# Kernel optimization log

Measured on AMD Instinct MI355X. Metric: run time of the kernel, lower is better.

Reference implementation:

```python
import jax, jax.numpy as jnp
import numpy as np

IN_DIM = 128
OUT_DIM = 128
H = 8
HD = OUT_DIM // H  # 16
EPS = 1e-5
NEG = -1e30


def setup_inputs() -> dict:
    key = jax.random.key(0)
    ks = jax.random.split(key, 10)
    B, N = 8, 1024
    h = jax.random.normal(ks[0], (B, N, IN_DIM), dtype=jnp.float32)
    adj_mask = jax.random.randint(ks[1], (B, N, N), 0, 2, dtype=jnp.int32)
    s = 1.0 / np.sqrt(IN_DIM)
    W = jax.random.normal(ks[2], (H, IN_DIM, HD), dtype=jnp.float32) * s
    a = jax.random.normal(ks[3], (H, 2 * HD), dtype=jnp.float32) * (1.0 / np.sqrt(2 * HD))
    ln1_g = jnp.ones((OUT_DIM,), jnp.float32)
    ln1_b = jnp.zeros((OUT_DIM,), jnp.float32)
    w1 = jax.random.normal(ks[4], (OUT_DIM, 2 * OUT_DIM), dtype=jnp.float32) * (1.0 / np.sqrt(OUT_DIM))
    b1 = jnp.zeros((2 * OUT_DIM,), jnp.float32)
    w2 = jax.random.normal(ks[5], (2 * OUT_DIM, OUT_DIM), dtype=jnp.float32) * (1.0 / np.sqrt(2 * OUT_DIM))
    b2 = jnp.zeros((OUT_DIM,), jnp.float32)
    ln2_g = jnp.ones((OUT_DIM,), jnp.float32)
    ln2_b = jnp.zeros((OUT_DIM,), jnp.float32)
    return dict(h=h, adj_mask=adj_mask, W=W, a=a, ln1_g=ln1_g, ln1_b=ln1_b,
                w1=w1, b1=b1, w2=w2, b2=b2, ln2_g=ln2_g, ln2_b=ln2_b)


def _layernorm(x, g, b):
    mu = jnp.mean(x, axis=-1, keepdims=True)
    var = jnp.mean(jnp.square(x - mu), axis=-1, keepdims=True)
    return (x - mu) * jax.lax.rsqrt(var + EPS) * g + b


def reference(h, adj_mask, W, a, ln1_g, ln1_b, w1, b1, w2, b2, ln2_g, ln2_b):
    B, N, _ = h.shape
    # Per-head projection: (B,H,N,HD)
    Wh = jnp.einsum('bni,hid->bhnd', h, W)
    # a.[Wh_i, Wh_j] = a_src.Wh_i + a_dst.Wh_j (decompose concat-score)
    a_src, a_dst = a[:, :HD], a[:, HD:]
    s_i = jnp.einsum('bhnd,hd->bhn', Wh, a_src)  # source term
    s_j = jnp.einsum('bhnd,hd->bhn', Wh, a_dst)  # target term
    e = s_i[:, :, :, None] + s_j[:, :, None, :]  # (B,H,N,N)
    e = jnp.where(e >= 0, e, 0.2 * e)            # LeakyReLU(0.2)
    mask = (adj_mask != 0)[:, None, :, :]        # (B,1,N,N)
    e = jnp.where(mask, e, NEG)
    alpha = jax.nn.softmax(e, axis=-1)
    # rows with no neighbors -> NaN in torch softmax -> zeroed; replicate
    row_valid = jnp.any(mask, axis=-1, keepdims=True)  # (B,1,N,1)
    alpha = jnp.where(row_valid, alpha, 0.0)
    # dropout in eval mode = identity
    h_heads = jnp.einsum('bhnm,bhmd->bhnd', alpha, Wh)
    h_cat = h_heads.transpose(0, 2, 1, 3).reshape(B, N, H * HD)
    # residual (in_dim == out_dim here)
    h_cat = _layernorm(h_cat + h, ln1_g, ln1_b)
    ffn = jnp.maximum(h_cat @ w1 + b1, 0.0) @ w2 + b2
    return _layernorm(h_cat + ffn, ln2_g, ln2_b)
```

## Files before the change

kernel.cpp:

```cpp
#include <hip/hip_runtime.h>
#include <hip/hip_bf16.h>

#define IN_DIM 128
#define OUT_DIM 128
#define NHEAD 8
#define HD 16
#define BB 8
#define NN 1024
#define LOG2E 1.44269504f

typedef unsigned long long u64;
typedef float f32x4 __attribute__((ext_vector_type(4)));
typedef short bf16x8 __attribute__((ext_vector_type(8)));

__global__ __launch_bounds__(256) void k_prep(
    const float* __restrict__ hin, const float* __restrict__ W,
    const float* __restrict__ a, const int* __restrict__ adj,
    unsigned* __restrict__ bits_t, unsigned short* __restrict__ whT,
    float* __restrict__ si_g, float* __restrict__ sj_g,
    const float* __restrict__ w1, const float* __restrict__ w2,
    unsigned short* __restrict__ w1T, unsigned short* __restrict__ w2T)
{
    __shared__ float smem[32 * 132];
    int blk = blockIdx.x;
    int t = threadIdx.x;

    if (blk < 256) {
        int b = blk >> 5, ntile = blk & 31;
        const float* hrow = hin + ((size_t)b * NN + ntile * 32) * IN_DIM;
#pragma unroll
        for (int it = 0; it < 4; ++it) {
            int g = t + 256 * it;
            int row = g >> 5, c4 = g & 31;
            float4 v = ((const float4*)hrow)[g];
            *(float4*)&smem[row * 132 + c4 * 4] = v;
        }
        __syncthreads();

        int d4 = t & 3;
        int hq = (t >> 2) & 7;
        int ngrp = t >> 5;
        float acc[4][4];
#pragma unroll
        for (int q = 0; q < 4; ++q)
#pragma unroll
            for (int dd = 0; dd < 4; ++dd) acc[q][dd] = 0.f;

        for (int i4 = 0; i4 < 32; ++i4) {
            float4 wf[4];
#pragma unroll
            for (int k = 0; k < 4; ++k)
                wf[k] = *(const float4*)&W[((size_t)hq * 128 + i4 * 4 + k) * 16 + d4 * 4];
            float4 hv[4];
#pragma unroll
            for (int q = 0; q < 4; ++q)
                hv[q] = *(const float4*)&smem[(ngrp * 4 + q) * 132 + i4 * 4];
#pragma unroll
            for (int q = 0; q < 4; ++q) {
                acc[q][0] += hv[q].x * wf[0].x + hv[q].y * wf[1].x + hv[q].z * wf[2].x + hv[q].w * wf[3].x;
                acc[q][1] += hv[q].x * wf[0].y + hv[q].y * wf[1].y + hv[q].z * wf[2].y + hv[q].w * wf[3].y;
                acc[q][2] += hv[q].x * wf[0].z + hv[q].y * wf[1].z + hv[q].z * wf[2].z + hv[q].w * wf[3].z;
                acc[q][3] += hv[q].x * wf[0].w + hv[q].y * wf[1].w + hv[q].z * wf[2].w + hv[q].w * wf[3].w;
            }
        }

        int bh = b * NHEAD + hq;
        int rowbase = ntile * 32 + ngrp * 4;

        float asrc[4], adst[4];
#pragma unroll
        for (int dd = 0; dd < 4; ++dd) {
            asrc[dd] = a[hq * 32 + d4 * 4 + dd];
            adst[dd] = a[hq * 32 + 16 + d4 * 4 + dd];
        }
#pragma unroll
        for (int q = 0; q < 4; ++q) {
            float psi = acc[q][0] * asrc[0] + acc[q][1] * asrc[1] + acc[q][2] * asrc[2] + acc[q][3] * asrc[3];
            float psj = acc[q][0] * adst[0] + acc[q][1] * adst[1] + acc[q][2] * adst[2] + acc[q][3] * adst[3];
            psi += __shfl_xor(psi, 1); psi += __shfl_xor(psi, 2);
            psj += __shfl_xor(psj, 1); psj += __shfl_xor(psj, 2);
            if (d4 == 0) {
                si_g[(size_t)bh * NN + rowbase + q] = psi * LOG2E;
                sj_g[(size_t)bh * NN + rowbase + q] = psj * LOG2E;
            }
        }

#pragma unroll
        for (int dd = 0; dd < 4; ++dd) {
            unsigned u0, u1;
            asm("v_cvt_pk_bf16_f32 %0, %1, %2" : "=v"(u0) : "v"(acc[0][dd]), "v"(acc[1][dd]));
            asm("v_cvt_pk_bf16_f32 %0, %1, %2" : "=v"(u1) : "v"(acc[2][dd]), "v"(acc[3][dd]));
            uint2 pk = make_uint2(u0, u1);
            *(uint2*)&whT[((size_t)bh * 16 + d4 * 4 + dd) * 1024 + rowbase] = pk;
        }
    } else if (blk < 2304) {
        int lane = t & 63;
        int wid = (blk - 256) * 4 + (t >> 6);
        for (int w = wid; w < BB * NN * 16; w += 2048 * 4) {
            int v = adj[(size_t)w * 64 + lane];
            u64 m = __ballot(v != 0);
            if (lane == 0) {
                int b = w >> 14, i = (w >> 4) & 1023, k = w & 15;
                unsigned* dst = bits_t + ((size_t)b * 32 + k * 2) * 1024 + i;
                dst[0] = (unsigned)m;
                dst[1024] = (unsigned)(m >> 32);
            }
        }
    } else {
        int bb = blk - 2304;
        const float* src; unsigned short* dst; int R, C;
        if (bb < 32) { src = w1; dst = w1T; R = 128; C = 256; }
        else         { src = w2; dst = w2T; R = 256; C = 128; bb -= 32; }
        int tpr = C >> 5;
        int tr = bb / tpr, tc = bb - tr * tpr;
        int r0 = tr << 5, c0 = tc << 5;
        int lr = t >> 5, lc = t & 31;
#pragma unroll
        for (int p = 0; p < 4; ++p)
            smem[(lr + p * 8) * 33 + lc] = src[(size_t)(r0 + lr + p * 8) * C + c0 + lc];
        __syncthreads();
#pragma unroll
        for (int p = 0; p < 4; ++p) {
            __hip_bfloat16 bv = __float2bfloat16(smem[lc * 33 + lr + p * 8]);
            dst[(size_t)(c0 + lr + p * 8) * R + r0 + lc] = *(unsigned short*)&bv;
        }
    }
}

__global__ __launch_bounds__(512, 3) void k_attn(
    const unsigned short* __restrict__ whT,
    const unsigned* __restrict__ bits_t,
    const float* __restrict__ si_g, const float* __restrict__ sj_g,
    float* __restrict__ hh)
{
    __shared__ __align__(16) unsigned short whT_s[16 * 1032];
    __shared__ __align__(16) float sj_s[NN];
    int t = threadIdx.x;
    int blk = blockIdx.x;
    int part = blk & 7;
    int bh = blk >> 3;
    int hq = bh & 7, b = bh >> 3;
    int blkrow = part * 128;

    {
        const uint4* src = (const uint4*)(whT + (size_t)bh * 16 * 1024);
#pragma unroll
        for (int it = 0; it < 4; ++it) {
            int g = t + 512 * it;
            int d = g >> 7, c8 = g & 127;
            uint4 v = src[g];
            *(uint4*)&whT_s[d * 1032 + c8 * 8] = v;
        }
        if (t < 256) *(float4*)&sj_s[t * 4] = ((const float4*)(sj_g + (size_t)bh * NN))[t];
    }
    __syncthreads();

    int wv = t >> 6, lane = t & 63;
    int lo16 = lane & 15, g = lane >> 4;
    int row = blkrow + wv * 16 + lo16;
    float si_r = si_g[(size_t)bh * NN + row];
    const unsigned* mcol = bits_t + (size_t)b * 32 * 1024 + row;

    f32x4 acc = {0.f, 0.f, 0.f, 0.f};
    float lsum = 0.f;
    unsigned m = mcol[0];
#pragma unroll 4
    for (int kt = 0; kt < 32; ++kt) {
        unsigned m_next = (kt < 31) ? mcol[(size_t)(kt + 1) * 1024] : 0u;
        bf16x8 bfrag = *(const bf16x8*)&whT_s[lo16 * 1032 + kt * 32 + g * 8];
        unsigned mm = m >> (g * 8);
        const float* sjp = &sj_s[kt * 32 + g * 8];
        union { bf16x8 v; unsigned u[4]; } af;
#pragma unroll
        for (int e2 = 0; e2 < 4; ++e2) {
            float v0 = si_r + sjp[2 * e2];
            float v1 = si_r + sjp[2 * e2 + 1];
            float lv0 = __builtin_fmaf(0.4f, __builtin_fabsf(v0), 0.6f * v0);
            float lv1 = __builtin_fmaf(0.4f, __builtin_fabsf(v1), 0.6f * v1);
            lv0 = ((mm >> (2 * e2)) & 1) ? lv0 : -150.f;
            lv1 = ((mm >> (2 * e2 + 1)) & 1) ? lv1 : -150.f;
            float p0, p1;
            asm("v_exp_f32 %0, %1" : "=v"(p0) : "v"(lv0));
            asm("v_exp_f32 %0, %1" : "=v"(p1) : "v"(lv1));
            lsum += p0 + p1;
            asm("v_cvt_pk_bf16_f32 %0, %1, %2" : "=v"(af.u[e2]) : "v"(p0), "v"(p1));
        }
        acc = __builtin_amdgcn_mfma_f32_16x16x32_bf16(af.v, bfrag, acc, 0, 0, 0);
        m = m_next;
    }

    lsum += __shfl_xor(lsum, 16);
    lsum += __shfl_xor(lsum, 32);

    float* obase = hh + ((size_t)b * NN + blkrow + wv * 16) * OUT_DIM + hq * HD + lo16;
#pragma unroll
    for (int q = 0; q < 4; ++q) {
        float ls = __shfl(lsum, 4 * g + q);
        float r = (ls > 0.f) ? 1.0f / ls : 0.f;
        obase[(size_t)(4 * g + q) * OUT_DIM] = acc[q] * r;
    }
}

__global__ __launch_bounds__(512, 1) void k_ffn(const float* __restrict__ hhs,
                                                const float* __restrict__ hin,
                                                const float* __restrict__ g1,
                                                const float* __restrict__ bt1,
                                                const unsigned short* __restrict__ w1T,
                                                const float* __restrict__ bb1,
                                                const unsigned short* __restrict__ w2T,
                                                const float* __restrict__ bb2,
                                                const float* __restrict__ g2,
                                                const float* __restrict__ bt2,
                                                float* __restrict__ out) {
    __shared__ float xc_f[32][128];
    __shared__ float y_f[32][132];
    __shared__ __align__(16) unsigned short xc_bf[32 * 128];
    __shared__ __align__(16) unsigned short hid_bf[32 * 256];

    int t = threadIdx.x;
    int R0 = blockIdx.x * 32;
    int wv = t >> 6, lane = t & 63;
    int lo = lane & 15, g = lane >> 4;

    bf16x8 b1f[2][4];
#pragma unroll
    for (int jt = 0; jt < 2; ++jt) {
        int n = (wv * 2 + jt) * 16 + lo;
#pragma unroll
        for (int kt = 0; kt < 4; ++kt)
            b1f[jt][kt] = *(const bf16x8*)&w1T[(size_t)n * 128 + kt * 32 + g * 8];
    }
    bf16x8 b2f[8];
    {
        int n = wv * 16 + lo;
#pragma unroll
        for (int kt = 0; kt < 8; ++kt)
            b2f[kt] = *(const bf16x8*)&w2T[(size_t)n * 256 + kt * 32 + g * 8];
    }
    float b1v[2];
    b1v[0] = bb1[(wv * 2 + 0) * 16 + lo];
    b1v[1] = bb1[(wv * 2 + 1) * 16 + lo];
    float b2v = bb2[wv * 16 + lo];

    {
        int r = t >> 4, c = t & 15;
        size_t row = (size_t)(R0 + r) * 128;
        float4 ha = *(const float4*)&hhs[row + c * 8];
        float4 hb = *(const float4*)&hhs[row + c * 8 + 4];
        float4 ia = *(const float4*)&hin[row + c * 8];
        float4 ib = *(const float4*)&hin[row + c * 8 + 4];
        float x[8] = {ha.x + ia.x, ha.y + ia.y, ha.z + ia.z, ha.w + ia.w,
                      hb.x + ib.x, hb.y + ib.y, hb.z + ib.z, hb.w + ib.w};
        float s = 0.f, s2 = 0.f;
#pragma unroll
        for (int j = 0; j < 8; ++j) { s += x[j]; s2 += x[j] * x[j]; }
#pragma unroll
        for (int off = 8; off > 0; off >>= 1) {
            s += __shfl_xor(s, off);
            s2 += __shfl_xor(s2, off);
        }
        float mu = s * (1.f / 128.f);
        float var = s2 * (1.f / 128.f) - mu * mu;
        float rs = rsqrtf(var + 1e-5f);
        float4 ga = *(const float4*)&g1[c * 8], gb = *(const float4*)&g1[c * 8 + 4];
        float4 ba = *(const float4*)&bt1[c * 8], bb = *(const float4*)&bt1[c * 8 + 4];
        float gg[8] = {ga.x, ga.y, ga.z, ga.w, gb.x, gb.y, gb.z, gb.w};
        float bbv[8] = {ba.x, ba.y, ba.z, ba.w, bb.x, bb.y, bb.z, bb.w};
        float xo[8];
#pragma unroll
        for (int j = 0; j < 8; ++j) xo[j] = (x[j] - mu) * rs * gg[j] + bbv[j];
        *(float4*)&xc_f[r][c * 8]     = make_float4(xo[0], xo[1], xo[2], xo[3]);
        *(float4*)&xc_f[r][c * 8 + 4] = make_float4(xo[4], xo[5], xo[6], xo[7]);
        union { uint4 v; unsigned u[4]; } pk;
#pragma unroll
        for (int q = 0; q < 4; ++q)
            asm("v_cvt_pk_bf16_f32 %0, %1, %2" : "=v"(pk.u[q]) : "v"(xo[2 * q]), "v"(xo[2 * q + 1]));
        int byte = (r * 256 + c * 16) ^ ((r & 7) << 4);
        *(uint4*)((char*)xc_bf + byte) = pk.v;
    }
    __syncthreads();

    {
        bf16x8 af[2][4];
#pragma unroll
        for (int mt = 0; mt < 2; ++mt) {
            int m = mt * 16 + lo;
#pragma unroll
            for (int kt = 0; kt < 4; ++kt) {
                int byte = (m * 256 + kt * 64 + g * 16) ^ ((m & 7) << 4);
                af[mt][kt] = *(const bf16x8*)((const char*)xc_bf + byte);
            }
        }
#pragma unroll
        for (int mt = 0; mt < 2; ++mt)
#pragma unroll
            for (int jt = 0; jt < 2; ++jt) {
                f32x4 acc = {0.f, 0.f, 0.f, 0.f};
#pragma unroll
                for (int kt = 0; kt < 4; ++kt)
                    acc = __builtin_amdgcn_mfma_f32_16x16x32_bf16(af[mt][kt], b1f[jt][kt], acc, 0, 0, 0);
                int n = (wv * 2 + jt) * 16 + lo;
#pragma unroll
                for (int q = 0; q < 4; ++q) {
                    float hv = fmaxf(acc[q] + b1v[jt], 0.f);
                    int m = mt * 16 + 4 * g + q;
                    int byte = (m * 512 + n * 2) ^ ((m & 7) << 4);
                    __hip_bfloat16 bv = __float2bfloat16(hv);
                    *(unsigned short*)((char*)hid_bf + byte) = *(unsigned short*)&bv;
                }
            }
    }
    __syncthreads();

    {
        f32x4 acc2[2] = {{0.f, 0.f, 0.f, 0.f}, {0.f, 0.f, 0.f, 0.f}};
#pragma unroll
        for (int mt = 0; mt < 2; ++mt) {
            int m = mt * 16 + lo;
#pragma unroll
            for (int kt = 0; kt < 8; ++kt) {
                int byte = (m * 512 + kt * 64 + g * 16) ^ ((m & 7) << 4);
                bf16x8 a = *(const bf16x8*)((const char*)hid_bf + byte);
                acc2[mt] = __builtin_amdgcn_mfma_f32_16x16x32_bf16(a, b2f[kt], acc2[mt], 0, 0, 0);
            }
        }
        int n = wv * 16 + lo;
#pragma unroll
        for (int mt = 0; mt < 2; ++mt)
#pragma unroll
            for (int q = 0; q < 4; ++q)
                y_f[mt * 16 + 4 * g + q][n] = acc2[mt][q] + b2v;
    }
    __syncthreads();

    {
        int r = t >> 4, c = t & 15;
        float xv[8];
        float s = 0.f, s2 = 0.f;
#pragma unroll
        for (int j = 0; j < 8; ++j) {
            float v = xc_f[r][c * 8 + j] + y_f[r][c * 8 + j];
            xv[j] = v; s += v; s2 += v * v;
        }
#pragma unroll
        for (int off = 8; off > 0; off >>= 1) {
            s += __shfl_xor(s, off);
            s2 += __shfl_xor(s2, off);
        }
        float mu = s * (1.f / 128.f);
        float var = s2 * (1.f / 128.f) - mu * mu;
        float rs = rsqrtf(var + 1e-5f);
        float4 ga = *(const float4*)&g2[c * 8], gb = *(const float4*)&g2[c * 8 + 4];
        float4 ba = *(const float4*)&bt2[c * 8], bb = *(const float4*)&bt2[c * 8 + 4];
        float o[8] = {(xv[0] - mu) * rs * ga.x + ba.x, (xv[1] - mu) * rs * ga.y + ba.y,
                      (xv[2] - mu) * rs * ga.z + ba.z, (xv[3] - mu) * rs * ga.w + ba.w,
                      (xv[4] - mu) * rs * gb.x + bb.x, (xv[5] - mu) * rs * gb.y + bb.y,
                      (xv[6] - mu) * rs * gb.z + bb.z, (xv[7] - mu) * rs * gb.w + bb.w};
        size_t row = (size_t)(R0 + r) * 128;
        *(float4*)&out[row + c * 8]     = make_float4(o[0], o[1], o[2], o[3]);
        *(float4*)&out[row + c * 8 + 4] = make_float4(o[4], o[5], o[6], o[7]);
    }
}

extern "C" void kernel_launch(void* const* d_in, const int* in_sizes, int n_in,
                              void* d_out, int out_size, void* d_ws, size_t ws_size,
                              hipStream_t stream) {
    const float* hin  = (const float*)d_in[0];
    const int*   adj  = (const int*)d_in[1];
    const float* W    = (const float*)d_in[2];
    const float* a    = (const float*)d_in[3];
    const float* ln1g = (const float*)d_in[4];
    const float* ln1b = (const float*)d_in[5];
    const float* w1   = (const float*)d_in[6];
    const float* b1   = (const float*)d_in[7];
    const float* w2   = (const float*)d_in[8];
    const float* b2   = (const float*)d_in[9];
    const float* ln2g = (const float*)d_in[10];
    const float* ln2b = (const float*)d_in[11];
    float* out = (float*)d_out;

    unsigned* bits_t    = (unsigned*)d_ws;
    unsigned short* whT = (unsigned short*)((char*)d_ws + (1u << 20));
    float* si_g         = (float*)((char*)d_ws + (3u << 20));
    float* sj_g         = (float*)((char*)d_ws + (3u << 20) + (256u << 10));
    float* hh           = (float*)((char*)d_ws + (3u << 20) + (512u << 10));
    unsigned short* w1T = (unsigned short*)((char*)d_ws + (7u << 20) + (512u << 10));
    unsigned short* w2T = (unsigned short*)((char*)d_ws + (7u << 20) + (512u << 10) + 65536);

    k_prep<<<2368, 256, 0, stream>>>(hin, W, a, adj, bits_t, whT, si_g, sj_g,
                                     w1, w2, w1T, w2T);
    k_attn<<<BB * NHEAD * 8, 512, 0, stream>>>(whT, bits_t, si_g, sj_g, hh);
    k_ffn<<<BB * NN / 32, 512, 0, stream>>>(hh, hin, ln1g, ln1b, w1T, b1, w2T, b2, ln2g, ln2b, out);
}
```

Baseline: 62.60 us.

## Factor LeakyReLU exponentials into per-row/per-column products and batch adjacency ballots

The attention kernel now precomputes exp(sj) and exp(0.2*sj) per column in shared memory and exp(si), exp(0.2*si) per row. Each score becomes max(e^si*e^sj, e^0.2si*e^0.2sj), which removes the per-element transcendental and the LeakyReLU arithmetic from the inner loop. The adjacency bit-packing loop also issues four independent loads and ballots per iteration so more memory accesses are in flight. The trade-offs are twice the shared-memory reads per element and a risk of overflow, since the exponentials are taken without subtracting a row maximum.

```diff
diff --git a/kernel.cpp b/kernel.cpp
--- a/kernel.cpp
+++ b/kernel.cpp
@@ -96,14 +96,31 @@
     } else if (blk < 2304) {
         int lane = t & 63;
         int wid = (blk - 256) * 4 + (t >> 6);
-        for (int w = wid; w < BB * NN * 16; w += 2048 * 4) {
-            int v = adj[(size_t)w * 64 + lane];
-            u64 m = __ballot(v != 0);
+#pragma unroll 1
+        for (int base = 0; base < 4; ++base) {
+            int w0 = wid + (base * 4 + 0) * 8192;
+            int w1v = wid + (base * 4 + 1) * 8192;
+            int w2v = wid + (base * 4 + 2) * 8192;
+            int w3v = wid + (base * 4 + 3) * 8192;
+            int v0 = adj[(size_t)w0 * 64 + lane];
+            int v1 = adj[(size_t)w1v * 64 + lane];
+            int v2 = adj[(size_t)w2v * 64 + lane];
+            int v3 = adj[(size_t)w3v * 64 + lane];
+            u64 m0 = __ballot(v0 != 0);
+            u64 m1 = __ballot(v1 != 0);
+            u64 m2 = __ballot(v2 != 0);
+            u64 m3 = __ballot(v3 != 0);
             if (lane == 0) {
-                int b = w >> 14, i = (w >> 4) & 1023, k = w & 15;
-                unsigned* dst = bits_t + ((size_t)b * 32 + k * 2) * 1024 + i;
-                dst[0] = (unsigned)m;
-                dst[1024] = (unsigned)(m >> 32);
+                int ws[4] = {w0, w1v, w2v, w3v};
+                u64 ms[4] = {m0, m1, m2, m3};
+#pragma unroll
+                for (int u = 0; u < 4; ++u) {
+                    int w = ws[u];
+                    int b = w >> 14, i = (w >> 4) & 1023, k = w & 15;
+                    unsigned* dst = bits_t + ((size_t)b * 32 + k * 2) * 1024 + i;
+                    dst[0] = (unsigned)ms[u];
+                    dst[1024] = (unsigned)(ms[u] >> 32);
+                }
             }
         }
     } else {
@@ -134,7 +151,8 @@
     float* __restrict__ hh)
 {
     __shared__ __align__(16) unsigned short whT_s[16 * 1032];
-    __shared__ __align__(16) float sj_s[NN];
+    __shared__ __align__(16) float ejp_s[NN];
+    __shared__ __align__(16) float ejn_s[NN];
     int t = threadIdx.x;
     int blk = blockIdx.x;
     int part = blk & 7;
@@ -151,44 +169,58 @@
             uint4 v = src[g];
             *(uint4*)&whT_s[d * 1032 + c8 * 8] = v;
         }
-        if (t < 256) *(float4*)&sj_s[t * 4] = ((const float4*)(sj_g + (size_t)bh * NN))[t];
+#pragma unroll
+        for (int jt = 0; jt < 2; ++jt) {
+            int j = t + jt * 512;
+            float sjv = sj_g[(size_t)bh * NN + j];
+            float ep, en;
+            asm("v_exp_f32 %0, %1" : "=v"(ep) : "v"(sjv));
+            asm("v_exp_f32 %0, %1" : "=v"(en) : "v"(0.2f * sjv));
+            ejp_s[j] = ep;
+            ejn_s[j] = en;
+        }
     }
     __syncthreads();
 
     int wv = t >> 6, lane = t & 63;
     int lo16 = lane & 15, g = lane >> 4;
     int row = blkrow + wv * 16 + lo16;
-    float si_r = si_g[(size_t)bh * NN + row];
+    float siL = si_g[(size_t)bh * NN + row];
+    float esip, esin;
+    asm("v_exp_f32 %0, %1" : "=v"(esip) : "v"(siL));
+    asm("v_exp_f32 %0, %1" : "=v"(esin) : "v"(0.2f * siL));
     const unsigned* mcol = bits_t + (size_t)b * 32 * 1024 + row;
 
     f32x4 acc = {0.f, 0.f, 0.f, 0.f};
-    float lsum = 0.f;
+    float lsA = 0.f, lsB = 0.f;
     unsigned m = mcol[0];
 #pragma unroll 4
     for (int kt = 0; kt < 32; ++kt) {
         unsigned m_next = (kt < 31) ? mcol[(size_t)(kt + 1) * 1024] : 0u;
         bf16x8 bfrag = *(const bf16x8*)&whT_s[lo16 * 1032 + kt * 32 + g * 8];
+        float4 pa = *(const float4*)&ejp_s[kt * 32 + g * 8];
+        float4 pb = *(const float4*)&ejp_s[kt * 32 + g * 8 + 4];
+        float4 na = *(const float4*)&ejn_s[kt * 32 + g * 8];
+        float4 nb = *(const float4*)&ejn_s[kt * 32 + g * 8 + 4];
         unsigned mm = m >> (g * 8);
-        const float* sjp = &sj_s[kt * 32 + g * 8];
+        float ep[8] = {pa.x, pa.y, pa.z, pa.w, pb.x, pb.y, pb.z, pb.w};
+        float en[8] = {na.x, na.y, na.z, na.w, nb.x, nb.y, nb.z, nb.w};
         union { bf16x8 v; unsigned u[4]; } af;
 #pragma unroll
         for (int e2 = 0; e2 < 4; ++e2) {
-            float v0 = si_r + sjp[2 * e2];
-            float v1 = si_r + sjp[2 * e2 + 1];
-            float lv0 = __builtin_fmaf(0.4f, __builtin_fabsf(v0), 0.6f * v0);
-            float lv1 = __builtin_fmaf(0.4f, __builtin_fabsf(v1), 0.6f * v1);
-            lv0 = ((mm >> (2 * e2)) & 1) ? lv0 : -150.f;
-            lv1 = ((mm >> (2 * e2 + 1)) & 1) ? lv1 : -150.f;
-            float p0, p1;
-            asm("v_exp_f32 %0, %1" : "=v"(p0) : "v"(lv0));
-            asm("v_exp_f32 %0, %1" : "=v"(p1) : "v"(lv1));
-            lsum += p0 + p1;
-            asm("v_cvt_pk_bf16_f32 %0, %1, %2" : "=v"(af.u[e2]) : "v"(p0), "v"(p1));
+            float q0 = fmaxf(esip * ep[2 * e2], esin * en[2 * e2]);
+            float q1 = fmaxf(esip * ep[2 * e2 + 1], esin * en[2 * e2 + 1]);
+            q0 = ((mm >> (2 * e2)) & 1) ? q0 : 0.f;
+            q1 = ((mm >> (2 * e2 + 1)) & 1) ? q1 : 0.f;
+            lsA += q0;
+            lsB += q1;
+            asm("v_cvt_pk_bf16_f32 %0, %1, %2" : "=v"(af.u[e2]) : "v"(q0), "v"(q1));
         }
         acc = __builtin_amdgcn_mfma_f32_16x16x32_bf16(af.v, bfrag, acc, 0, 0, 0);
         m = m_next;
     }
 
+    float lsum = lsA + lsB;
     lsum += __shfl_xor(lsum, 16);
     lsum += __shfl_xor(lsum, 32);
 
```

Result: no change. 62.01 us (-0.9%).
